# Optimization experiments

Hardware: AMD Instinct MI355X
Metric: run time of the kernel (lower is better)

The kernel has to match this reference:

```python
import jax, jax.numpy as jnp
import numpy as np

N_BITS = 8
IN_FEATURES = 2048
OUT_FEATURES = 512
BATCH = 8
THRESHOLD = 0.5


def setup_inputs() -> dict:
    key = jax.random.key(0)
    kx, kw = jax.random.split(key)
    x = jax.random.uniform(kx, (BATCH, IN_FEATURES), dtype=jnp.float32)
    # nn.init.normal_(weight, mean=0.5, std=1.0) then clamp_(0, 1)
    weight = 0.5 + jax.random.normal(kw, (IN_FEATURES, OUT_FEATURES * N_BITS), dtype=jnp.float32)
    weight = jnp.clip(weight, 0.0, 1.0)
    return {"x": x, "weight": weight}


def _carry_save_adder(addends):
    # addends: [M, F, n_bits] -> reduce over F via full-adder chain.
    # Bit index 0 = LSB; carry shifts one position toward MSB each step.
    M, F, nb = addends.shape
    a_seq = jnp.transpose(addends, (1, 0, 2))  # [F, M, nb]
    init = (jnp.zeros((M, nb), addends.dtype), jnp.zeros((M, nb), addends.dtype))

    def step(state, a):
        s, c = state
        t = s + a + c
        half = jnp.floor(t * 0.5)          # carry bit (zero-gradient)
        sum_b = t - 2.0 * half             # t mod 2 (identity gradient w.r.t. t)
        c_next = jnp.pad(half[:, :-1], ((0, 0), (1, 0)))  # shift-left: LSB carry-in = 0
        return (sum_b, c_next), None

    (s, c), _ = jax.lax.scan(step, init, a_seq)
    return s, c


def reference(x, weight):
    # STE binarization of the weights (forward value = hard bits)
    w = jnp.clip(weight, 0.0, 1.0)
    hard = w + jax.lax.stop_gradient((w >= THRESHOLD).astype(w.dtype) - w)
    # [B, F, 1] * [1, F, O*nb] -> [B, F, O*nb]
    ff = x[:, :, None] * hard[None, :, :]
    B, F, _ = ff.shape
    O = ff.shape[-1] // N_BITS
    # split(n_bits, dim=-1) + stack(dim=-3) + reshape -> [B*O, F, n_bits]
    stacked = ff.reshape(B, F, O, N_BITS).transpose(0, 2, 1, 3).reshape(B * O, F, N_BITS)
    s, carry = _carry_save_adder(stacked)   # [B*O, nb], [B*O, nb]
    s = s.reshape(B, N_BITS * O)
    return (s, carry)
```

## Files before the change

kernel.cpp:

```cpp
#include <hip/hip_runtime.h>


#define F_DIM 2048
#define K_DIM 4096
#define B_DIM 8
#define G     32
#define NG    (F_DIM / G)
#define NB2   4

#define PK_BYTES (64 * NG * 64 * 4)

__device__ __forceinline__ float dpp_row_shr1(float v) {
    int r = __builtin_amdgcn_update_dpp(0, __float_as_int(v), 0x111, 0xf, 0xf, true);
    return __int_as_float(r);
}

__device__ __forceinline__ int sext_bit(unsigned bits, int u) {
#if __has_builtin(__builtin_amdgcn_sbfe)
    return __builtin_amdgcn_sbfe((int)bits, (unsigned)u, 1u);
#else
    return ((int)(bits << (31 - u))) >> 31;
#endif
}

__global__ __launch_bounds__(64) void pack_kernel(const float* __restrict__ w,
                                                  unsigned* __restrict__ pk) {
    const int lane = threadIdx.x;
    const int og   = blockIdx.x;
    const int f32  = blockIdx.y;
    const float* wp = w + og * 64 + lane;
    unsigned bits = 0;
#pragma unroll
    for (int j = 0; j < 32; ++j) {
        float wv = wp[(f32 * 32 + j) * K_DIM];
        bits |= (wv >= 0.5f ? 1u : 0u) << j;
    }
    pk[(og * 64 + f32) * 64 + lane] = bits;
}

__global__ __launch_bounds__(64, 1) void csa_main(const float* __restrict__ x,
                                                  const unsigned* __restrict__ pk,
                                                  float* __restrict__ out) {
    const int lane = threadIdx.x;
    const int og   = blockIdx.x + 8 * blockIdx.y;
    const int b    = blockIdx.z;
    const int k    = og * 64 + lane;

    const float kmask = ((lane & 7) == 7) ? 0.0f : 1.0f;

    int zero;
    asm volatile("v_mov_b32 %0, 0" : "=v"(zero));

    const unsigned* bp  = pk + og * (NG * 64) + lane;
    const float4*   xp4 = (const float4*)(x + b * F_DIM) + zero;

    unsigned bbuf[NB2];
    float4   xb[NB2][G / 4];

#pragma unroll
    for (int p = 0; p < NB2; ++p) {
        bbuf[p] = bp[p * 64];
#pragma unroll
        for (int q = 0; q < G / 4; ++q)
            xb[p][q] = xp4[p * (G / 4) + q];
    }

    float s = 0.0f, c = 0.0f;

    for (int g0 = 0; g0 < NG; g0 += NB2) {
#pragma unroll
        for (int p = 0; p < NB2; ++p) {
            const float*   xf   = (const float*)&xb[p][0];
            const unsigned bits = bbuf[p];
#pragma unroll
            for (int u = 0; u < G; ++u) {
                int   m  = sext_bit(bits, u);
                float a  = __int_as_float(m & __float_as_int(xf[u]));
                float uu = s + a;
                float t  = uu + c;
                bool  ge = (t >= 2.0f);
                float h  = ge ? kmask : 0.0f;
                s = ge ? (t - 2.0f) : t;
                c = dpp_row_shr1(h);
            }
            int gb = g0 + p + NB2;
            int gc = (gb < NG) ? gb : (NG - 1);
            bbuf[p] = bp[gc * 64];
#pragma unroll
            for (int q = 0; q < G / 4; ++q)
                xb[p][q] = xp4[gc * (G / 4) + q];
        }
    }

    out[b * K_DIM + k]                 = s;
    out[B_DIM * K_DIM + b * K_DIM + k] = c;
}

#define U_FB  16
#define NB_FB 4
__global__ __launch_bounds__(64, 1) void csa_fallback(const float* __restrict__ x,
                                                      const float* __restrict__ weight,
                                                      float* __restrict__ out) {
    const int lane = threadIdx.x;
    const int og   = blockIdx.x + 8 * blockIdx.y;
    const int b    = blockIdx.z;
    const int k    = og * 64 + lane;
    const float kmask = ((lane & 7) == 7) ? 0.0f : 1.0f;
    int zero;
    asm volatile("v_mov_b32 %0, 0" : "=v"(zero));
    const float*  wp  = weight + k;
    const float4* xp4 = (const float4*)(x + b * F_DIM) + zero;
    float  wb[NB_FB][U_FB];
    float4 xb[NB_FB][U_FB / 4];
#pragma unroll
    for (int p = 0; p < NB_FB; ++p) {
#pragma unroll
        for (int u = 0; u < U_FB; ++u) wb[p][u] = wp[(p * U_FB + u) * K_DIM];
#pragma unroll
        for (int q = 0; q < U_FB / 4; ++q) xb[p][q] = xp4[(p * U_FB) / 4 + q];
    }
    float s = 0.0f, c = 0.0f;
    for (int f0 = 0; f0 < F_DIM; f0 += NB_FB * U_FB) {
#pragma unroll
        for (int p = 0; p < NB_FB; ++p) {
            const float* xf = (const float*)&xb[p][0];
#pragma unroll
            for (int u = 0; u < U_FB; ++u) {
                float a  = (wb[p][u] >= 0.5f) ? xf[u] : 0.0f;
                float uu = s + a;
                float t  = uu + c;
                bool  ge = (t >= 2.0f);
                float h  = ge ? kmask : 0.0f;
                s = ge ? (t - 2.0f) : t;
                c = dpp_row_shr1(h);
            }
            int fb = f0 + p * U_FB + NB_FB * U_FB;
            int fc = (fb <= F_DIM - U_FB) ? fb : (F_DIM - U_FB);
#pragma unroll
            for (int u = 0; u < U_FB; ++u) wb[p][u] = wp[(fc + u) * K_DIM];
#pragma unroll
            for (int q = 0; q < U_FB / 4; ++q) xb[p][q] = xp4[fc / 4 + q];
        }
    }
    out[b * K_DIM + k]                 = s;
    out[B_DIM * K_DIM + b * K_DIM + k] = c;
}

extern "C" void kernel_launch(void* const* d_in, const int* in_sizes, int n_in,
                              void* d_out, int out_size, void* d_ws, size_t ws_size,
                              hipStream_t stream) {
    (void)in_sizes; (void)n_in; (void)out_size;
    const float* x      = (const float*)d_in[0];
    const float* weight = (const float*)d_in[1];
    float* out          = (float*)d_out;

    if (ws_size >= (size_t)PK_BYTES && d_ws != nullptr) {
        unsigned* pk = (unsigned*)d_ws;
        pack_kernel<<<dim3(64, 64, 1), dim3(64), 0, stream>>>(weight, pk);
        csa_main<<<dim3(8, 8, 8), dim3(64), 0, stream>>>(x, pk, out);
    } else {
        csa_fallback<<<dim3(8, 8, 8), dim3(64), 0, stream>>>(x, weight, out);
    }
}
```

Baseline: 125.5 us.

## Distribute x across lanes and broadcast with readlane; defer carry shift

Each lane now loads one x value per 64-feature superblock, and values are broadcast with v_readlane into scalar registers. This replaces every lane loading the same 32 floats as float4 vectors, cutting vector register pressure and redundant loads. The DPP carry shift is moved to the start of each step, which takes it off the s-to-t dependency tail and adds one final shift after the loop. Double-buffered prefetch of two superblocks is kept. readlane puts scalar reads in the hot loop, and the serial dependency chain still sets the pace.

Result: faster. 114.4 us (-8.9%).

```diff
diff --git a/kernel.cpp b/kernel.cpp
--- a/kernel.cpp
+++ b/kernel.cpp
@@ -6,7 +6,7 @@
 #define B_DIM 8
 #define G     32
 #define NG    (F_DIM / G)
-#define NB2   4
+#define NSB   (F_DIM / 64)
 
 #define PK_BYTES (64 * NG * 64 * 4)
 
@@ -48,52 +48,53 @@
 
     const float kmask = ((lane & 7) == 7) ? 0.0f : 1.0f;
 
-    int zero;
-    asm volatile("v_mov_b32 %0, 0" : "=v"(zero));
+    const unsigned* bp = pk + og * (NG * 64) + lane;
+    const int*      xp = (const int*)(x + b * F_DIM) + lane;
 
-    const unsigned* bp  = pk + og * (NG * 64) + lane;
-    const float4*   xp4 = (const float4*)(x + b * F_DIM) + zero;
+    unsigned pkA0 = bp[0 * 64], pkA1 = bp[1 * 64];
+    int      xA   = xp[0 * 64];
+    unsigned pkB0 = bp[2 * 64], pkB1 = bp[3 * 64];
+    int      xB   = xp[1 * 64];
 
-    unsigned bbuf[NB2];
-    float4   xb[NB2][G / 4];
+    float s = 0.0f;
+    float h = 0.0f;
 
-#pragma unroll
-    for (int p = 0; p < NB2; ++p) {
-        bbuf[p] = bp[p * 64];
-#pragma unroll
-        for (int q = 0; q < G / 4; ++q)
-            xb[p][q] = xp4[p * (G / 4) + q];
+#define STEP64(PK0, PK1, XV)                                              \
+    _Pragma("unroll")                                                      \
+    for (int u = 0; u < 64; ++u) {                                         \
+        int      xs   = __builtin_amdgcn_readlane((XV), u);                \
+        unsigned bits = (u < 32) ? (PK0) : (PK1);                          \
+        int      m    = sext_bit(bits, u & 31);                            \
+        float    a    = __int_as_float(m & xs);     \
+        float    cn   = dpp_row_shr1(h);           \
+        float    uu   = s + a;                            \
+        float    t    = uu + cn;                                           \
+        bool     ge   = (t >= 2.0f);                                       \
+        h = ge ? kmask : 0.0f;                                             \
+        s = ge ? (t - 2.0f) : t;                                           \
     }
 
-    float s = 0.0f, c = 0.0f;
-
-    for (int g0 = 0; g0 < NG; g0 += NB2) {
-#pragma unroll
-        for (int p = 0; p < NB2; ++p) {
-            const float*   xf   = (const float*)&xb[p][0];
-            const unsigned bits = bbuf[p];
-#pragma unroll
-            for (int u = 0; u < G; ++u) {
-                int   m  = sext_bit(bits, u);
-                float a  = __int_as_float(m & __float_as_int(xf[u]));
-                float uu = s + a;
-                float t  = uu + c;
-                bool  ge = (t >= 2.0f);
-                float h  = ge ? kmask : 0.0f;
-                s = ge ? (t - 2.0f) : t;
-                c = dpp_row_shr1(h);
-            }
-            int gb = g0 + p + NB2;
-            int gc = (gb < NG) ? gb : (NG - 1);
-            bbuf[p] = bp[gc * 64];
-#pragma unroll
-            for (int q = 0; q < G / 4; ++q)
-                xb[p][q] = xp4[gc * (G / 4) + q];
+    for (int sb = 0; sb < NSB; sb += 2) {
+        STEP64(pkA0, pkA1, xA);
+        {
+            int nsb = sb + 2; int csb = (nsb < NSB) ? nsb : (NSB - 2);
+            pkA0 = bp[(2 * csb + 0) * 64];
+            pkA1 = bp[(2 * csb + 1) * 64];
+            xA   = xp[csb * 64];
+        }
+        STEP64(pkB0, pkB1, xB);
+        {
+            int nsb = sb + 3; int csb = (nsb < NSB) ? nsb : (NSB - 2);
+            pkB0 = bp[(2 * csb + 0) * 64];
+            pkB1 = bp[(2 * csb + 1) * 64];
+            xB   = xp[csb * 64];
         }
     }
+#undef STEP64
 
+    float cfin = dpp_row_shr1(h);
     out[b * K_DIM + k]                 = s;
-    out[B_DIM * K_DIM + b * K_DIM + k] = c;
+    out[B_DIM * K_DIM + b * K_DIM + k] = cfin;
 }
 
 #define U_FB  16
@@ -130,9 +131,9 @@
                 float uu = s + a;
                 float t  = uu + c;
                 bool  ge = (t >= 2.0f);
-                float h  = ge ? kmask : 0.0f;
+                float hh = ge ? kmask : 0.0f;
                 s = ge ? (t - 2.0f) : t;
-                c = dpp_row_shr1(h);
+                c = dpp_row_shr1(hh);
             }
             int fb = f0 + p * U_FB + NB_FB * U_FB;
             int fc = (fb <= F_DIM - U_FB) ? fb : (F_DIM - U_FB);
```
